# Kernel tuning notes

Measured on AMD Instinct MI355X. Metric: run time of the kernel, lower is better.

The kernel has to match this reference:

```python
import jax, jax.numpy as jnp
import numpy as np

H = 128          # hidden_size
GX = GY = 512    # grid_size
SW = 2           # spatial_width
NX = GX + 3 * SW # memory extent x (as in SpatialExternalMemory ctor)
NY = GY + 3 * SW
B = 512          # batch (num trajectories)
T = 64           # seq len (recurrent steps)


def setup_inputs() -> dict:
    key = jax.random.key(0)
    ks = jax.random.split(key, 9)
    stdv = 1.0 / np.sqrt(H)
    feat = jax.random.normal(ks[0], (B, T, 2), jnp.float32)
    # integer grid coords stored as floats in cols 2:4 (cast to long in forward)
    coords = jax.random.randint(ks[1], (B, T, 2), 0, GX).astype(jnp.float32)
    feature_tensor = jnp.concatenate([feat, coords], axis=-1)  # [B, T, 4]
    seq_lengths = jax.random.randint(ks[2], (B,), 1, T + 1)
    uni = lambda k, shp: jax.random.uniform(k, shp, jnp.float32, -stdv, stdv)
    return {
        "feature_tensor": feature_tensor,
        "W_ih": uni(ks[3], (4 * H, 2)),
        "b_ih": uni(ks[4], (4 * H,)),
        "W_hh": uni(ks[5], (4 * H, H)),
        "b_hh": uni(ks[6], (4 * H,)),
        "W_out": uni(ks[7], (H, 2 * H)),   # Attention.linear_out: [H, 2H]
        "b_out": uni(ks[8], (H,)),
        "seq_lengths": seq_lengths,
    }


def reference(feature_tensor, W_ih, b_ih, W_hh, b_hh, W_out, b_out, seq_lengths):
    step_idx = jnp.maximum(seq_lengths.astype(jnp.int32), 1) - 1  # [B]
    offsets = jnp.arange(-SW, SW + 1)                              # [K], K=2*SW+1
    K = 2 * SW + 1
    memory0 = jnp.zeros((NX, NY, H), jnp.float32)
    hidden0 = jnp.zeros((B, H), jnp.float32)
    last0 = jnp.zeros((B, H), jnp.float32)

    def step(carry, inp):
        hidden, memory, last = carry
        xt, t = inp                                 # xt: [B,4]
        feat = xt[:, :2]
        grid = xt[:, 2:4].astype(jnp.int32) + SW    # [B,2]
        gi = feat @ W_ih.T + b_ih                   # [B,4H]
        gh = hidden @ W_hh.T + b_hh                 # [B,4H]
        i_r, i_i, i_n, i_s = jnp.split(gi, 4, axis=1)
        h_r, h_i, h_n, h_s = jnp.split(gh, 4, axis=1)
        resetgate = jax.nn.sigmoid(i_r + h_r)
        updategate = jax.nn.sigmoid(i_i + h_i)
        spatialgate = jax.nn.sigmoid(i_s + h_s)
        newgate = jnp.tanh(i_n + resetgate * h_n)
        # --- find_nearby_grids: 5x5 neighborhood gather ---
        gx = jnp.clip(grid[:, 0], 0, NX - 1)
        gy = jnp.clip(grid[:, 1], 0, NY - 1)
        xi = jnp.clip(gx[:, None] + offsets[None, :], 0, NX - 1)   # [B,K]
        yi = jnp.clip(gy[:, None] + offsets[None, :], 0, NY - 1)   # [B,K]
        xg = jnp.broadcast_to(xi[:, :, None], (B, K, K)).reshape(B, K * K)
        yg = jnp.broadcast_to(yi[:, None, :], (B, K, K)).reshape(B, K * K)
        context = memory[xg, yg]                    # [B, K*K, H]
        # --- Attention(newgate.detach(), context) ---
        q = jax.lax.stop_gradient(newgate)
        scores = jnp.einsum('bh,bkh->bk', q, context)
        scores = jnp.where(scores == 0.0, -jnp.inf, scores)
        attn = jax.nn.softmax(scores, axis=1)
        attn = jnp.where(jnp.isnan(attn), 0.0, attn)
        mix = jnp.einsum('bk,bkh->bh', attn, context)
        atten_cs = jnp.tanh(jnp.concatenate([mix, q], axis=-1) @ W_out.T + b_out)
        curr = newgate + spatialgate * atten_cs
        out = curr + updategate * (hidden - curr)
        # --- in-cell memory write (detached, training-mode path) ---
        sd = jax.lax.stop_gradient(spatialgate)
        od = jax.lax.stop_gradient(out)
        upd = sd * memory[gx, gy] + (1.0 - sd) * od
        memory = memory.at[gx, gy].set(upd)
        last = jnp.where((step_idx == t)[:, None], out, last)
        return (out, memory, last), None

    xs = (jnp.swapaxes(feature_tensor, 0, 1), jnp.arange(T))
    (_, _, last), _ = jax.lax.scan(step, (hidden0, memory0, last0), xs)
    return last
```

## Files before the change

### kernel.cpp

```cpp
#include <hip/hip_runtime.h>
#include <hip/hip_fp16.h>
#include <math.h>

#define Hc   128
#define Bc   512
#define Tc   64
#define NXc  518
#define NCELL (518*518)
#define NEV  (Bc*Tc)
#define SWc  2


__global__ void k_build(const float* __restrict__ feat, int* __restrict__ head,
                        int* __restrict__ nxt, int* __restrict__ cellxy) {
    int gid = blockIdx.x * 256 + threadIdx.x;
    if (gid >= NEV) return;
    int b = gid >> 6, t = gid & 63;
    int base = (b * Tc + t) * 4;
    int gx = (int)feat[base + 2] + SWc;
    int gy = (int)feat[base + 3] + SWc;
    gx = min(max(gx, 0), NXc - 1);
    gy = min(max(gy, 0), NXc - 1);
    int cell = gx * NXc + gy;
    int e = t * Bc + b;
    cellxy[e] = (gx << 16) | gy;
    int old = atomicExch(&head[cell], e);
    nxt[e] = old;
}

__global__ void k_resolve(const int* __restrict__ head, const int* __restrict__ nxt,
                          const int* __restrict__ cellxy, int* __restrict__ dep) {
    int gid = blockIdx.x * 256 + threadIdx.x;
    if (gid >= NEV * 25) return;
    int r = gid / 25, k = gid - r * 25;
    int t = r & 63, b = r >> 6;
    int e0 = t * Bc + b;
    int xy = cellxy[e0];
    int gx = xy >> 16, gy = xy & 0xffff;
    int cx = gx + (k / 5) - SWc, cy = gy + (k % 5) - SWc;
    cx = min(max(cx, 0), NXc - 1);
    cy = min(max(cy, 0), NXc - 1);
    int cell = cx * NXc + cy;
    int best = -1;
    for (int e = head[cell]; e >= 0; e = nxt[e])
        if ((e >> 9) < t && e > best) best = e;
    dep[r * 25 + k] = best;
}


#define LOG2E 1.4426950408889634f
__device__ __forceinline__ float fexp(float x)  { return __builtin_amdgcn_exp2f(x * LOG2E); }
__device__ __forceinline__ float fsig(float x)  { return __builtin_amdgcn_rcpf(1.f + fexp(-x)); }
__device__ __forceinline__ float ftanh(float x) { return 1.f - 2.f * __builtin_amdgcn_rcpf(1.f + fexp(2.f * x)); }

template <int CTRL>
__device__ __forceinline__ float dppadd(float x) {
    int t = __builtin_amdgcn_update_dpp(0, __float_as_int(x), CTRL, 0xF, 0xF, true);
    return x + __int_as_float(t);
}
template <int CTRL>
__device__ __forceinline__ float dppmax(float x) {
    int t = __builtin_amdgcn_update_dpp(0, __float_as_int(x), CTRL, 0xF, 0xF, true);
    return fmaxf(x, __int_as_float(t));
}
__device__ __forceinline__ float swz16(float x) {
    return __int_as_float(__builtin_amdgcn_ds_swizzle(__float_as_int(x), 0x401F));
}
__device__ __forceinline__ float redsum64(float d) {
    d = dppadd<0xB1>(d); d = dppadd<0x4E>(d);
    d = dppadd<0x141>(d); d = dppadd<0x140>(d);
    d += swz16(d);
    d += __shfl_xor(d, 32, 64);
    return d;
}

__device__ __forceinline__ void barlds() {
    asm volatile("" ::: "memory");
    __builtin_amdgcn_s_waitcnt(0xC07F);
    __builtin_amdgcn_s_barrier();
    asm volatile("" ::: "memory");
}


constexpr int LDS_FLOATS = 16512 + 256 + 1024 + 256 + 256 + 256 + 64 + 2048 + 512 + 16 + 128 + 256 + 128;
constexpr int LDS_BYTES  = LDS_FLOATS * 4;

__global__ void
__attribute__((amdgpu_flat_work_group_size(1024, 1024)))
__attribute__((amdgpu_waves_per_eu(4, 4)))
step_main(const float* __restrict__ feat, const float* __restrict__ Wih,
          const float* __restrict__ bih,  const float* __restrict__ Whh,
          const float* __restrict__ bhh,  const float* __restrict__ Wout,
          const float* __restrict__ bout, const int*   __restrict__ seq,
          const int*   __restrict__ dep,  float* __restrict__ vbuf,
          unsigned*    __restrict__ flags, float* __restrict__ dout) {
    extern __shared__ float lds[];
    __half2* WoutH = (__half2*)lds;
    float* hid   = lds + 16512;
    float* g     = hid   + 256;
    float* gin   = g     + 1024;
    float* ctr   = gin   + 256;
    float* qvL   = ctr   + 256;
    float* scor  = qvL   + 256;
    float* pmix  = scor  + 64;
    float* catL  = pmix  + 2048;
    float* fxy   = catL  + 512;
    float* boutL = fxy   + 16;
    float* updL  = boutL + 128;
    int*   depv  = (int*)(updL + 256);

    const int tid  = threadIdx.x;
    const int blk  = blockIdx.x;
    const int lane = tid & 63;
    const int w    = tid >> 6;
    const int wj   = w >> 3;
    const int ww   = w & 7;

    const int rp = tid >> 2;
    const int q  = tid & 3;
    const int r0 = 2 * rp, r1 = 2 * rp + 1;
    float4 wr0[8], wr1[8];
    {
        const float4* w0 = (const float4*)(Whh + (size_t)r0 * Hc);
        const float4* w1 = (const float4*)(Whh + (size_t)r1 * Hc);
        #pragma unroll
        for (int i = 0; i < 8; ++i) { wr0[i] = w0[q + 4 * i]; wr1[i] = w1[q + 4 * i]; }
    }
    #pragma unroll
    for (int i = 0; i < 8; ++i) {
        asm volatile("" : "+v"(wr0[i].x), "+v"(wr0[i].y), "+v"(wr0[i].z), "+v"(wr0[i].w));
        asm volatile("" : "+v"(wr1[i].x), "+v"(wr1[i].y), "+v"(wr1[i].z), "+v"(wr1[i].w));
    }
    const int jw = q & 1;
    const int rw = r0 + (q >> 1);
    const float bihr = bih[rw], bhhr = bhh[rw];
    const float wihA = Wih[rw * 2 + 0], wihB = Wih[rw * 2 + 1];
    const int chunk = rw >> 7;

    for (int i = tid; i < 128 * 128; i += 1024) {
        int r = i >> 7, c2 = i & 127;
        WoutH[r * 129 + c2] = __floats2half2_rn(Wout[r * 256 + 2 * c2],
                                                Wout[r * 256 + 2 * c2 + 1]);
    }
    if (tid < 128) boutL[tid] = bout[tid];
    if (tid < 256) hid[tid] = 0.f;
    if (tid < 8) { int j = tid >> 2, c = tid & 3;
                   fxy[tid] = feat[((size_t)(blk * 2 + j) * Tc + 0) * 4 + c]; }
    if (tid < 50) {
        int j = (tid >= 25), k = tid - j * 25;
        depv[tid] = dep[(((size_t)(blk * 2 + j)) * Tc + 0) * 25 + k];
    }
    const int s0 = max(seq[blk * 2 + 0], 1) - 1;
    const int s1 = max(seq[blk * 2 + 1], 1) - 1;
    __syncthreads();

    const float NEG_INF = -__builtin_inff();

    for (int t = 0; t < Tc; ++t) {
        const float* fx = fxy + (t & 1) * 8;
        int* depvCur = depv + (t & 1) * 64;
        int* depvNxt = depv + ((t + 1) & 1) * 64;

        if (t > 0 && (w == 0 || w == 2)) {
            int j = w >> 1;
            float2 u = *(const float2*)&updL[j * 128 + 2 * lane];
            unsigned long long raw; __builtin_memcpy(&raw, &u, 8);
            __hip_atomic_store((unsigned long long*)(vbuf +
                ((size_t)((t - 1) * Bc + blk * 2 + j)) * Hc + 2 * lane),
                raw, __ATOMIC_RELAXED, __HIP_MEMORY_SCOPE_AGENT);
        }
        const int mye = (lane < 25) ? depvCur[wj * 25 + lane] : -1;
        unsigned fpre = 1u;
        if (mye >= 0)
            fpre = __hip_atomic_load(&flags[mye], __ATOMIC_RELAXED,
                                     __HIP_MEMORY_SCOPE_AGENT);

        float a00 = 0.f, a01 = 0.f, a10 = 0.f, a11 = 0.f;
        {
            const float4* h0 = (const float4*)hid;
            const float4* h1 = (const float4*)(hid + 128);
            #pragma unroll
            for (int i = 0; i < 8; ++i) {
                float4 hv0 = h0[q + 4 * i], hv1 = h1[q + 4 * i];
                float4 w0 = wr0[i], w1 = wr1[i];
                a00 = fmaf(w0.x, hv0.x, fmaf(w0.y, hv0.y, fmaf(w0.z, hv0.z, fmaf(w0.w, hv0.w, a00))));
                a01 = fmaf(w1.x, hv0.x, fmaf(w1.y, hv0.y, fmaf(w1.z, hv0.z, fmaf(w1.w, hv0.w, a01))));
                a10 = fmaf(w0.x, hv1.x, fmaf(w0.y, hv1.y, fmaf(w0.z, hv1.z, fmaf(w0.w, hv1.w, a10))));
                a11 = fmaf(w1.x, hv1.x, fmaf(w1.y, hv1.y, fmaf(w1.z, hv1.z, fmaf(w1.w, hv1.w, a11))));
            }
        }
        a00 = dppadd<0x4E>(dppadd<0xB1>(a00));
        a01 = dppadd<0x4E>(dppadd<0xB1>(a01));
        a10 = dppadd<0x4E>(dppadd<0xB1>(a10));
        a11 = dppadd<0x4E>(dppadd<0xB1>(a11));
        {
            float mine = (q & 1) ? ((q >> 1) ? a11 : a10) : ((q >> 1) ? a01 : a00);
            float gi  = fmaf(wihA, fx[jw * 4 + 0], wihB * fx[jw * 4 + 1]);
            g[jw * 512 + rw] = mine + bhhr + ((chunk == 2) ? 0.f : (gi + bihr));
            if (chunk == 2) gin[jw * 128 + (rw & 127)] = gi + bihr;
        }
        if (tid >= 512 && tid < 562 && t + 1 < Tc) {
            int idx = tid - 512;
            int j = (idx >= 25), k = idx - j * 25;
            depvNxt[idx] = dep[(((size_t)(blk * 2 + j)) * Tc + (t + 1)) * 25 + k];
        }
        if (tid >= 960 && tid < 968 && t + 1 < Tc) {
            int idx = tid - 960, j = idx >> 2, c = idx & 3;
            fxy[((t + 1) & 1) * 8 + idx] =
                feat[((size_t)(blk * 2 + j) * Tc + (t + 1)) * 4 + c];
        }
        if (t > 0 && (w == 0 || w == 2)) {
            asm volatile("s_waitcnt vmcnt(0)" ::: "memory");
            if (lane == 0)
                __hip_atomic_store(&flags[(t - 1) * Bc + blk * 2 + (w >> 1)], 1u,
                                   __ATOMIC_RELAXED, __HIP_MEMORY_SCOPE_AGENT);
        }
        {
            bool pend = (mye >= 0) && (fpre == 0u);
            while (__any(pend)) {
                if (pend && __hip_atomic_load(&flags[mye], __ATOMIC_RELAXED,
                                              __HIP_MEMORY_SCOPE_AGENT) != 0u)
                    pend = false;
                if (__any(pend)) __builtin_amdgcn_s_sleep(1);
            }
        }
        asm volatile("" ::: "memory");
        float2 valk[4];
        int    evk[4];
        #pragma unroll
        for (int kk = 0; kk < 4; ++kk) {
            int k = ww + 8 * kk;
            evk[kk] = (k < 25) ? depvCur[wj * 25 + k] : -1;
            valk[kk] = make_float2(0.f, 0.f);
            if (evk[kk] >= 0)
                valk[kk] = *(const float2*)(vbuf + (size_t)evk[kk] * Hc + 2 * lane);
        }
        barlds();

        float q0, q1;
        {
            float2 gr2 = *(const float2*)&g[wj * 512 + 2 * lane];
            float2 gn2 = *(const float2*)&g[wj * 512 + 256 + 2 * lane];
            float2 gi2 = *(const float2*)&gin[wj * 128 + 2 * lane];
            q0 = ftanh(gi2.x + fsig(gr2.x) * gn2.x);
            q1 = ftanh(gi2.y + fsig(gr2.y) * gn2.y);
        }
        if (ww == 0) *(float2*)&qvL[wj * 128 + 2 * lane] = make_float2(q0, q1);
        if (ww == 4)
            *(float2*)&ctr[wj * 128 + 2 * lane] =
                (evk[1] >= 0) ? valk[1] : make_float2(0.f, 0.f);
        #pragma unroll
        for (int kk = 0; kk < 4; ++kk) {
            int k = ww + 8 * kk;
            if (k < 25) {
                float sc;
                if (evk[kk] >= 0) {
                    float d = fmaf(valk[kk].x, q0, valk[kk].y * q1);
                    d = redsum64(d);
                    sc = (d == 0.f) ? NEG_INF : d;
                } else sc = NEG_INF;
                if (lane == 0) scor[wj * 32 + k] = sc;
            }
        }
        barlds();

        {
            int k2 = lane & 31;
            float v = (k2 < 25) ? scor[wj * 32 + k2] : NEG_INF;
            float m = v;
            m = dppmax<0xB1>(m); m = dppmax<0x4E>(m);
            m = dppmax<0x141>(m); m = dppmax<0x140>(m);
            m = fmaxf(m, swz16(m));
            float a = 0.f;
            if (m != NEG_INF) {
                float p = (v == NEG_INF) ? 0.f : fexp(v - m);
                float s = p;
                s = dppadd<0xB1>(s); s = dppadd<0x4E>(s);
                s = dppadd<0x141>(s); s = dppadd<0x140>(s);
                s += swz16(s);
                a = p / s;
            }
            float pm0 = 0.f, pm1 = 0.f;
            #pragma unroll
            for (int kk = 0; kk < 4; ++kk) {
                int k = ww + 8 * kk;
                if (k < 25 && evk[kk] >= 0) {
                    float ak = __int_as_float(
                        __builtin_amdgcn_readlane(__float_as_int(a), k));
                    pm0 = fmaf(ak, valk[kk].x, pm0);
                    pm1 = fmaf(ak, valk[kk].y, pm1);
                }
            }
            *(float2*)&pmix[(wj * 8 + ww) * 128 + 2 * lane] = make_float2(pm0, pm1);
        }
        barlds();

        if (tid < 256) {
            int j = tid >> 7, h = tid & 127;
            float mix = 0.f;
            #pragma unroll
            for (int p = 0; p < 8; ++p) mix += pmix[(j * 8 + p) * 128 + h];
            catL[j * 256 + h] = mix;
            catL[j * 256 + 128 + h] = qvL[j * 128 + h];
        }
        barlds();

        {
            int oo = tid & 127, rep = tid >> 7;
            const __half2* wrow = WoutH + oo * 129 + rep * 16;
            const float4* c04 = (const float4*)(catL + rep * 32);
            const float4* c14 = (const float4*)(catL + 256 + rep * 32);
            float acc0 = 0.f, acc1 = 0.f;
            #pragma unroll
            for (int i = 0; i < 8; ++i) {
                __half2 wa = wrow[2 * i], wb = wrow[2 * i + 1];
                float wx = __low2float(wa), wy = __high2float(wa);
                float wz = __low2float(wb), wwv = __high2float(wb);
                float4 c0 = c04[i], c1 = c14[i];
                acc0 = fmaf(wx, c0.x, fmaf(wy, c0.y, fmaf(wz, c0.z, fmaf(wwv, c0.w, acc0))));
                acc1 = fmaf(wx, c1.x, fmaf(wy, c1.y, fmaf(wz, c1.z, fmaf(wwv, c1.w, acc1))));
            }
            pmix[rep * 128 + oo]       = acc0;
            pmix[(8 + rep) * 128 + oo] = acc1;
        }
        barlds();

        if (tid < 256) {
            int j = tid >> 7, h = tid & 127;
            float tot = boutL[h];
            #pragma unroll
            for (int p = 0; p < 8; ++p) tot += pmix[(j * 8 + p) * 128 + h];
            float at = ftanh(tot);
            float gr = g[j * 512 + h],       gu = g[j * 512 + 128 + h];
            float gn = g[j * 512 + 256 + h], gs = g[j * 512 + 384 + h];
            float rr = fsig(gr), uu = fsig(gu), ss = fsig(gs);
            float nn = ftanh(gin[j * 128 + h] + rr * gn);
            float hv = hid[j * 128 + h];
            float curr = fmaf(ss, at, nn);
            float outv = curr + uu * (hv - curr);
            hid[j * 128 + h] = outv;
            if (t < Tc - 1)
                updL[tid] = fmaf(ss, ctr[j * 128 + h], (1.f - ss) * outv);
            int sj = (j == 0) ? s0 : s1;
            if (sj == t) dout[(size_t)(blk * 2 + j) * Hc + h] = outv;
        }
        barlds();
    }
}


extern "C" void kernel_launch(void* const* d_in, const int* in_sizes, int n_in,
                              void* d_out, int out_size, void* d_ws, size_t ws_size,
                              hipStream_t stream) {
    const float* feat = (const float*)d_in[0];
    const float* Wih  = (const float*)d_in[1];
    const float* bih  = (const float*)d_in[2];
    const float* Whh  = (const float*)d_in[3];
    const float* bhh  = (const float*)d_in[4];
    const float* Wout = (const float*)d_in[5];
    const float* bout = (const float*)d_in[6];
    const int*   seq  = (const int*)d_in[7];

    char* ws = (char*)d_ws;
    size_t off = 0;
    auto carve = [&](size_t bytes) { char* p = ws + off; off += (bytes + 511) & ~(size_t)511; return p; };
    float*    vbuf   = (float*)   carve((size_t)NEV * Hc * 4);
    int*      head   = (int*)     carve((size_t)NCELL * 4);
    int*      nxt    = (int*)     carve((size_t)NEV * 4);
    int*      cellxy = (int*)     carve((size_t)NEV * 4);
    int*      dep    = (int*)     carve((size_t)NEV * 25 * 4);
    unsigned* flags  = (unsigned*)carve((size_t)NEV * 4);

    hipMemsetAsync(head, 0xFF, (size_t)NCELL * 4, stream);
    hipMemsetAsync(flags, 0, (size_t)NEV * 4, stream);

    k_build<<<(NEV + 255) / 256, 256, 0, stream>>>(feat, head, nxt, cellxy);
    k_resolve<<<(NEV * 25 + 255) / 256, 256, 0, stream>>>(head, nxt, cellxy, dep);

    hipFuncSetAttribute((const void*)step_main,
                        hipFuncAttributeMaxDynamicSharedMemorySize, LDS_BYTES);
    step_main<<<256, 1024, LDS_BYTES, stream>>>(feat, Wih, bih, Whh, bhh, Wout, bout,
                                                seq, dep, vbuf, flags, (float*)d_out);
}
```

Measured before the change: 459.1 us.

## Tag memory-update values with step counter to replace separate flag synchronization

Each published memory update now packs the float with a step tag in a 64-bit word, so consumers poll the data itself instead of a separate flag array. This removes the store-then-waitcnt-then-flag handshake and the extra flag load round trip. The output projection is reorganized so each wave computes 8 outputs with cross-lane reductions, and the mix partials are accumulated with LDS atomics, which eliminates two barriers and the pmix/qvL buffers. In exchange vbuf doubles in size and needs a full memset, and each published value is written with per-element 64-bit atomic stores.

```diff
diff --git a/kernel.cpp b/kernel.cpp
--- a/kernel.cpp
+++ b/kernel.cpp
@@ -81,8 +81,12 @@
     asm volatile("" ::: "memory");
 }
 
-
-constexpr int LDS_FLOATS = 16512 + 256 + 1024 + 256 + 256 + 256 + 64 + 2048 + 512 + 16 + 128 + 256 + 128;
+__device__ __forceinline__ unsigned long long gload(const unsigned long long* p) {
+    return __hip_atomic_load(p, __ATOMIC_RELAXED, __HIP_MEMORY_SCOPE_AGENT);
+}
+
+
+constexpr int LDS_FLOATS = 16512 + 256 + 1024 + 256 + 256 + 64 + 512 + 16 + 128 + 128;
 constexpr int LDS_BYTES  = LDS_FLOATS * 4;
 
 __global__ void
@@ -92,22 +96,19 @@
           const float* __restrict__ bih,  const float* __restrict__ Whh,
           const float* __restrict__ bhh,  const float* __restrict__ Wout,
           const float* __restrict__ bout, const int*   __restrict__ seq,
-          const int*   __restrict__ dep,  float* __restrict__ vbuf,
-          unsigned*    __restrict__ flags, float* __restrict__ dout) {
+          const int*   __restrict__ dep,  unsigned long long* __restrict__ vbuf,
+          float* __restrict__ dout) {
     extern __shared__ float lds[];
     __half2* WoutH = (__half2*)lds;
     float* hid   = lds + 16512;
     float* g     = hid   + 256;
     float* gin   = g     + 1024;
     float* ctr   = gin   + 256;
-    float* qvL   = ctr   + 256;
-    float* scor  = qvL   + 256;
-    float* pmix  = scor  + 64;
-    float* catL  = pmix  + 2048;
+    float* scor  = ctr   + 256;
+    float* catL  = scor  + 64;
     float* fxy   = catL  + 512;
     float* boutL = fxy   + 16;
-    float* updL  = boutL + 128;
-    int*   depv  = (int*)(updL + 256);
+    int*   depv  = (int*)(boutL + 128);
 
     const int tid  = threadIdx.x;
     const int blk  = blockIdx.x;
@@ -161,19 +162,17 @@
         int* depvCur = depv + (t & 1) * 64;
         int* depvNxt = depv + ((t + 1) & 1) * 64;
 
-        if (t > 0 && (w == 0 || w == 2)) {
-            int j = w >> 1;
-            float2 u = *(const float2*)&updL[j * 128 + 2 * lane];
-            unsigned long long raw; __builtin_memcpy(&raw, &u, 8);
-            __hip_atomic_store((unsigned long long*)(vbuf +
-                ((size_t)((t - 1) * Bc + blk * 2 + j)) * Hc + 2 * lane),
-                raw, __ATOMIC_RELAXED, __HIP_MEMORY_SCOPE_AGENT);
-        }
-        const int mye = (lane < 25) ? depvCur[wj * 25 + lane] : -1;
-        unsigned fpre = 1u;
-        if (mye >= 0)
-            fpre = __hip_atomic_load(&flags[mye], __ATOMIC_RELAXED,
-                                     __HIP_MEMORY_SCOPE_AGENT);
+        int evk[4]; unsigned long long g0[4], g1[4];
+        #pragma unroll
+        for (int kk = 0; kk < 4; ++kk) {
+            int k = ww + 8 * kk;
+            evk[kk] = (k < 25) ? depvCur[wj * 25 + k] : -1;
+            g0[kk] = 0; g1[kk] = 0;
+            if (evk[kk] >= 0) {
+                const unsigned long long* p = vbuf + ((size_t)evk[kk] << 7) + 2 * lane;
+                g0[kk] = gload(p); g1[kk] = gload(p + 1);
+            }
+        }
 
         float a00 = 0.f, a01 = 0.f, a10 = 0.f, a11 = 0.f;
         {
@@ -209,31 +208,34 @@
             fxy[((t + 1) & 1) * 8 + idx] =
                 feat[((size_t)(blk * 2 + j) * Tc + (t + 1)) * 4 + c];
         }
-        if (t > 0 && (w == 0 || w == 2)) {
-            asm volatile("s_waitcnt vmcnt(0)" ::: "memory");
-            if (lane == 0)
-                __hip_atomic_store(&flags[(t - 1) * Bc + blk * 2 + (w >> 1)], 1u,
-                                   __ATOMIC_RELAXED, __HIP_MEMORY_SCOPE_AGENT);
-        }
-        {
-            bool pend = (mye >= 0) && (fpre == 0u);
-            while (__any(pend)) {
-                if (pend && __hip_atomic_load(&flags[mye], __ATOMIC_RELAXED,
-                                              __HIP_MEMORY_SCOPE_AGENT) != 0u)
-                    pend = false;
-                if (__any(pend)) __builtin_amdgcn_s_sleep(1);
-            }
-        }
-        asm volatile("" ::: "memory");
-        float2 valk[4];
-        int    evk[4];
+        float2 valk[4]; bool pend[4];
         #pragma unroll
         for (int kk = 0; kk < 4; ++kk) {
-            int k = ww + 8 * kk;
-            evk[kk] = (k < 25) ? depvCur[wj * 25 + k] : -1;
-            valk[kk] = make_float2(0.f, 0.f);
-            if (evk[kk] >= 0)
-                valk[kk] = *(const float2*)(vbuf + (size_t)evk[kk] * Hc + 2 * lane);
+            pend[kk] = false; valk[kk] = make_float2(0.f, 0.f);
+            if (evk[kk] >= 0) {
+                unsigned exp = (unsigned)((evk[kk] >> 9) + 1);
+                valk[kk] = make_float2(__uint_as_float((unsigned)g0[kk]),
+                                       __uint_as_float((unsigned)g1[kk]));
+                pend[kk] = ((unsigned)(g0[kk] >> 32) != exp) ||
+                           ((unsigned)(g1[kk] >> 32) != exp);
+            }
+        }
+        while (__any(pend[0] | pend[1] | pend[2] | pend[3])) {
+            #pragma unroll
+            for (int kk = 0; kk < 4; ++kk) {
+                if (pend[kk]) {
+                    unsigned exp = (unsigned)((evk[kk] >> 9) + 1);
+                    const unsigned long long* p = vbuf + ((size_t)evk[kk] << 7) + 2 * lane;
+                    unsigned long long r0v = gload(p), r1v = gload(p + 1);
+                    if ((unsigned)(r0v >> 32) == exp && (unsigned)(r1v >> 32) == exp) {
+                        valk[kk] = make_float2(__uint_as_float((unsigned)r0v),
+                                               __uint_as_float((unsigned)r1v));
+                        pend[kk] = false;
+                    }
+                }
+            }
+            if (__any(pend[0] | pend[1] | pend[2] | pend[3]))
+                __builtin_amdgcn_s_sleep(1);
         }
         barlds();
 
@@ -245,7 +247,8 @@
             q0 = ftanh(gi2.x + fsig(gr2.x) * gn2.x);
             q1 = ftanh(gi2.y + fsig(gr2.y) * gn2.y);
         }
-        if (ww == 0) *(float2*)&qvL[wj * 128 + 2 * lane] = make_float2(q0, q1);
+        if (ww == 0) *(float2*)&catL[wj * 256 + 128 + 2 * lane] = make_float2(q0, q1);
+        if (ww == 1) *(float2*)&catL[wj * 256 + 2 * lane] = make_float2(0.f, 0.f);
         if (ww == 4)
             *(float2*)&ctr[wj * 128 + 2 * lane] =
                 (evk[1] >= 0) ? valk[1] : make_float2(0.f, 0.f);
@@ -280,69 +283,69 @@
                 s += swz16(s);
                 a = p / s;
             }
-            float pm0 = 0.f, pm1 = 0.f;
-            #pragma unroll
-            for (int kk = 0; kk < 4; ++kk) {
-                int k = ww + 8 * kk;
-                if (k < 25 && evk[kk] >= 0) {
-                    float ak = __int_as_float(
-                        __builtin_amdgcn_readlane(__float_as_int(a), k));
-                    pm0 = fmaf(ak, valk[kk].x, pm0);
-                    pm1 = fmaf(ak, valk[kk].y, pm1);
+            if ((evk[0] >= 0) | (evk[1] >= 0) | (evk[2] >= 0) | (evk[3] >= 0)) {
+                float pm0 = 0.f, pm1 = 0.f;
+                #pragma unroll
+                for (int kk = 0; kk < 4; ++kk) {
+                    int k = ww + 8 * kk;
+                    if (k < 25 && evk[kk] >= 0) {
+                        float ak = __int_as_float(
+                            __builtin_amdgcn_readlane(__float_as_int(a), k));
+                        pm0 = fmaf(ak, valk[kk].x, pm0);
+                        pm1 = fmaf(ak, valk[kk].y, pm1);
+                    }
                 }
-            }
-            *(float2*)&pmix[(wj * 8 + ww) * 128 + 2 * lane] = make_float2(pm0, pm1);
+                atomicAdd(&catL[wj * 256 + 2 * lane],     pm0);
+                atomicAdd(&catL[wj * 256 + 2 * lane + 1], pm1);
+            }
         }
         barlds();
 
-        if (tid < 256) {
-            int j = tid >> 7, h = tid & 127;
-            float mix = 0.f;
-            #pragma unroll
-            for (int p = 0; p < 8; ++p) mix += pmix[(j * 8 + p) * 128 + h];
-            catL[j * 256 + h] = mix;
-            catL[j * 256 + 128 + h] = qvL[j * 128 + h];
-        }
-        barlds();
-
-        {
-            int oo = tid & 127, rep = tid >> 7;
-            const __half2* wrow = WoutH + oo * 129 + rep * 16;
-            const float4* c04 = (const float4*)(catL + rep * 32);
-            const float4* c14 = (const float4*)(catL + 256 + rep * 32);
+        {
+            const int oi = lane & 7, p = lane >> 3;
+            const int oo = 8 * w + oi;
+            const __half2* wrow = WoutH + oo * 129 + p * 16;
+            const float4* cat4 = (const float4*)catL;
             float acc0 = 0.f, acc1 = 0.f;
             #pragma unroll
-            for (int i = 0; i < 8; ++i) {
-                __half2 wa = wrow[2 * i], wb = wrow[2 * i + 1];
+            for (int c = 0; c < 8; ++c) {
+                int cc = (c + p) & 7;
+                __half2 wa = wrow[2 * cc], wb = wrow[2 * cc + 1];
                 float wx = __low2float(wa), wy = __high2float(wa);
-                float wz = __low2float(wb), wwv = __high2float(wb);
-                float4 c0 = c04[i], c1 = c14[i];
-                acc0 = fmaf(wx, c0.x, fmaf(wy, c0.y, fmaf(wz, c0.z, fmaf(wwv, c0.w, acc0))));
-                acc1 = fmaf(wx, c1.x, fmaf(wy, c1.y, fmaf(wz, c1.z, fmaf(wwv, c1.w, acc1))));
-            }
-            pmix[rep * 128 + oo]       = acc0;
-            pmix[(8 + rep) * 128 + oo] = acc1;
-        }
-        barlds();
-
-        if (tid < 256) {
-            int j = tid >> 7, h = tid & 127;
-            float tot = boutL[h];
-            #pragma unroll
-            for (int p = 0; p < 8; ++p) tot += pmix[(j * 8 + p) * 128 + h];
-            float at = ftanh(tot);
-            float gr = g[j * 512 + h],       gu = g[j * 512 + 128 + h];
-            float gn = g[j * 512 + 256 + h], gs = g[j * 512 + 384 + h];
-            float rr = fsig(gr), uu = fsig(gu), ss = fsig(gs);
-            float nn = ftanh(gin[j * 128 + h] + rr * gn);
-            float hv = hid[j * 128 + h];
-            float curr = fmaf(ss, at, nn);
-            float outv = curr + uu * (hv - curr);
-            hid[j * 128 + h] = outv;
-            if (t < Tc - 1)
-                updL[tid] = fmaf(ss, ctr[j * 128 + h], (1.f - ss) * outv);
-            int sj = (j == 0) ? s0 : s1;
-            if (sj == t) dout[(size_t)(blk * 2 + j) * Hc + h] = outv;
+                float wz = __low2float(wb), wv = __high2float(wb);
+                float4 v0 = cat4[p * 8 + cc];
+                float4 v1 = cat4[64 + p * 8 + cc];
+                acc0 = fmaf(wx, v0.x, fmaf(wy, v0.y, fmaf(wz, v0.z, fmaf(wv, v0.w, acc0))));
+                acc1 = fmaf(wx, v1.x, fmaf(wy, v1.y, fmaf(wz, v1.z, fmaf(wv, v1.w, acc1))));
+            }
+            acc0 = dppadd<0x128>(acc0); acc0 += swz16(acc0); acc0 += __shfl_xor(acc0, 32, 64);
+            acc1 = dppadd<0x128>(acc1); acc1 += swz16(acc1); acc1 += __shfl_xor(acc1, 32, 64);
+            if (lane < 8) {
+                #pragma unroll
+                for (int j = 0; j < 2; ++j) {
+                    float tot = ((j == 0) ? acc0 : acc1) + boutL[oo];
+                    float at = ftanh(tot);
+                    float gr = g[j * 512 + oo],       gu = g[j * 512 + 128 + oo];
+                    float gn = g[j * 512 + 256 + oo], gs = g[j * 512 + 384 + oo];
+                    float rr = fsig(gr), uu = fsig(gu), ss = fsig(gs);
+                    float nn = ftanh(gin[j * 128 + oo] + rr * gn);
+                    float hv = hid[j * 128 + oo];
+                    float curr = fmaf(ss, at, nn);
+                    float outv = curr + uu * (hv - curr);
+                    hid[j * 128 + oo] = outv;
+                    if (t < Tc - 1) {
+                        float upd = fmaf(ss, ctr[j * 128 + oo], (1.f - ss) * outv);
+                        int e = t * Bc + blk * 2 + j;
+                        unsigned long long payload =
+                            ((unsigned long long)(unsigned)(t + 1) << 32) |
+                            (unsigned long long)__float_as_uint(upd);
+                        __hip_atomic_store(vbuf + ((size_t)e << 7) + oo, payload,
+                                           __ATOMIC_RELAXED, __HIP_MEMORY_SCOPE_AGENT);
+                    }
+                    int sj = (j == 0) ? s0 : s1;
+                    if (sj == t) dout[(size_t)(blk * 2 + j) * Hc + oo] = outv;
+                }
+            }
         }
         barlds();
     }
@@ -364,15 +367,14 @@
     char* ws = (char*)d_ws;
     size_t off = 0;
     auto carve = [&](size_t bytes) { char* p = ws + off; off += (bytes + 511) & ~(size_t)511; return p; };
-    float*    vbuf   = (float*)   carve((size_t)NEV * Hc * 4);
-    int*      head   = (int*)     carve((size_t)NCELL * 4);
-    int*      nxt    = (int*)     carve((size_t)NEV * 4);
-    int*      cellxy = (int*)     carve((size_t)NEV * 4);
-    int*      dep    = (int*)     carve((size_t)NEV * 25 * 4);
-    unsigned* flags  = (unsigned*)carve((size_t)NEV * 4);
-
+    unsigned long long* vbuf = (unsigned long long*)carve((size_t)NEV * Hc * 8);
+    int* head   = (int*)carve((size_t)NCELL * 4);
+    int* nxt    = (int*)carve((size_t)NEV * 4);
+    int* cellxy = (int*)carve((size_t)NEV * 4);
+    int* dep    = (int*)carve((size_t)NEV * 25 * 4);
+
+    hipMemsetAsync(vbuf, 0, (size_t)NEV * Hc * 8, stream);
     hipMemsetAsync(head, 0xFF, (size_t)NCELL * 4, stream);
-    hipMemsetAsync(flags, 0, (size_t)NEV * 4, stream);
 
     k_build<<<(NEV + 255) / 256, 256, 0, stream>>>(feat, head, nxt, cellxy);
     k_resolve<<<(NEV * 25 + 255) / 256, 256, 0, stream>>>(head, nxt, cellxy, dep);
@@ -380,5 +382,5 @@
     hipFuncSetAttribute((const void*)step_main,
                         hipFuncAttributeMaxDynamicSharedMemorySize, LDS_BYTES);
     step_main<<<256, 1024, LDS_BYTES, stream>>>(feat, Wih, bih, Whh, bhh, Wout, bout,
-                                                seq, dep, vbuf, flags, (float*)d_out);
-}
+                                                seq, dep, vbuf, (float*)d_out);
+}
```

New measurement: 933.0 us. 2.03x slower.

## Fuse attention mix and output projection phases, cutting per-step barriers

Applied to the files above, without the earlier changes.

Partial attention mixes are now accumulated straight into the concat buffer with LDS atomics instead of being staged in a separate buffer and summed later. The output projection is regrouped so each wave owns 8 output rows, with the K dimension split across lanes and reduced through DPP and swizzle. This lets the gate/update epilogue run in the same phase. Together these drop two block-wide barriers and two LDS staging buffers from every recurrent step. In exchange the code adds LDS atomics, a cross-lane reduction, and an epilogue that only 8 lanes per wave execute, which lowers parallelism in that stage.

```diff
diff --git a/kernel.cpp b/kernel.cpp
--- a/kernel.cpp
+++ b/kernel.cpp
@@ -82,7 +82,7 @@
 }
 
 
-constexpr int LDS_FLOATS = 16512 + 256 + 1024 + 256 + 256 + 256 + 64 + 2048 + 512 + 16 + 128 + 256 + 128;
+constexpr int LDS_FLOATS = 16512 + 256 + 1024 + 256 + 256 + 64 + 512 + 16 + 128 + 256 + 128;
 constexpr int LDS_BYTES  = LDS_FLOATS * 4;
 
 __global__ void
@@ -100,10 +100,8 @@
     float* g     = hid   + 256;
     float* gin   = g     + 1024;
     float* ctr   = gin   + 256;
-    float* qvL   = ctr   + 256;
-    float* scor  = qvL   + 256;
-    float* pmix  = scor  + 64;
-    float* catL  = pmix  + 2048;
+    float* scor  = ctr   + 256;
+    float* catL  = scor  + 64;
     float* fxy   = catL  + 512;
     float* boutL = fxy   + 16;
     float* updL  = boutL + 128;
@@ -245,7 +243,8 @@
             q0 = ftanh(gi2.x + fsig(gr2.x) * gn2.x);
             q1 = ftanh(gi2.y + fsig(gr2.y) * gn2.y);
         }
-        if (ww == 0) *(float2*)&qvL[wj * 128 + 2 * lane] = make_float2(q0, q1);
+        if (ww == 0) *(float2*)&catL[wj * 256 + 128 + 2 * lane] = make_float2(q0, q1);
+        if (ww == 1) *(float2*)&catL[wj * 256 + 2 * lane] = make_float2(0.f, 0.f);
         if (ww == 4)
             *(float2*)&ctr[wj * 128 + 2 * lane] =
                 (evk[1] >= 0) ? valk[1] : make_float2(0.f, 0.f);
@@ -280,69 +279,62 @@
                 s += swz16(s);
                 a = p / s;
             }
-            float pm0 = 0.f, pm1 = 0.f;
-            #pragma unroll
-            for (int kk = 0; kk < 4; ++kk) {
-                int k = ww + 8 * kk;
-                if (k < 25 && evk[kk] >= 0) {
-                    float ak = __int_as_float(
-                        __builtin_amdgcn_readlane(__float_as_int(a), k));
-                    pm0 = fmaf(ak, valk[kk].x, pm0);
-                    pm1 = fmaf(ak, valk[kk].y, pm1);
+            if ((evk[0] >= 0) | (evk[1] >= 0) | (evk[2] >= 0) | (evk[3] >= 0)) {
+                float pm0 = 0.f, pm1 = 0.f;
+                #pragma unroll
+                for (int kk = 0; kk < 4; ++kk) {
+                    int k = ww + 8 * kk;
+                    if (k < 25 && evk[kk] >= 0) {
+                        float ak = __int_as_float(
+                            __builtin_amdgcn_readlane(__float_as_int(a), k));
+                        pm0 = fmaf(ak, valk[kk].x, pm0);
+                        pm1 = fmaf(ak, valk[kk].y, pm1);
+                    }
                 }
-            }
-            *(float2*)&pmix[(wj * 8 + ww) * 128 + 2 * lane] = make_float2(pm0, pm1);
+                atomicAdd(&catL[wj * 256 + 2 * lane],     pm0);
+                atomicAdd(&catL[wj * 256 + 2 * lane + 1], pm1);
+            }
         }
         barlds();
 
-        if (tid < 256) {
-            int j = tid >> 7, h = tid & 127;
-            float mix = 0.f;
-            #pragma unroll
-            for (int p = 0; p < 8; ++p) mix += pmix[(j * 8 + p) * 128 + h];
-            catL[j * 256 + h] = mix;
-            catL[j * 256 + 128 + h] = qvL[j * 128 + h];
-        }
-        barlds();
-
-        {
-            int oo = tid & 127, rep = tid >> 7;
-            const __half2* wrow = WoutH + oo * 129 + rep * 16;
-            const float4* c04 = (const float4*)(catL + rep * 32);
-            const float4* c14 = (const float4*)(catL + 256 + rep * 32);
+        {
+            const int oi = lane & 7, p = lane >> 3;
+            const int oo = 8 * w + oi;
+            const __half2* wrow = WoutH + oo * 129 + p * 16;
+            const float4* cat4 = (const float4*)catL;
             float acc0 = 0.f, acc1 = 0.f;
             #pragma unroll
-            for (int i = 0; i < 8; ++i) {
-                __half2 wa = wrow[2 * i], wb = wrow[2 * i + 1];
+            for (int c = 0; c < 8; ++c) {
+                int cc = (c + p) & 7;
+                __half2 wa = wrow[2 * cc], wb = wrow[2 * cc + 1];
                 float wx = __low2float(wa), wy = __high2float(wa);
-                float wz = __low2float(wb), wwv = __high2float(wb);
-                float4 c0 = c04[i], c1 = c14[i];
-                acc0 = fmaf(wx, c0.x, fmaf(wy, c0.y, fmaf(wz, c0.z, fmaf(wwv, c0.w, acc0))));
-                acc1 = fmaf(wx, c1.x, fmaf(wy, c1.y, fmaf(wz, c1.z, fmaf(wwv, c1.w, acc1))));
-            }
-            pmix[rep * 128 + oo]       = acc0;
-            pmix[(8 + rep) * 128 + oo] = acc1;
-        }
-        barlds();
-
-        if (tid < 256) {
-            int j = tid >> 7, h = tid & 127;
-            float tot = boutL[h];
-            #pragma unroll
-            for (int p = 0; p < 8; ++p) tot += pmix[(j * 8 + p) * 128 + h];
-            float at = ftanh(tot);
-            float gr = g[j * 512 + h],       gu = g[j * 512 + 128 + h];
-            float gn = g[j * 512 + 256 + h], gs = g[j * 512 + 384 + h];
-            float rr = fsig(gr), uu = fsig(gu), ss = fsig(gs);
-            float nn = ftanh(gin[j * 128 + h] + rr * gn);
-            float hv = hid[j * 128 + h];
-            float curr = fmaf(ss, at, nn);
-            float outv = curr + uu * (hv - curr);
-            hid[j * 128 + h] = outv;
-            if (t < Tc - 1)
-                updL[tid] = fmaf(ss, ctr[j * 128 + h], (1.f - ss) * outv);
-            int sj = (j == 0) ? s0 : s1;
-            if (sj == t) dout[(size_t)(blk * 2 + j) * Hc + h] = outv;
+                float wz = __low2float(wb), wv = __high2float(wb);
+                float4 v0 = cat4[p * 8 + cc];
+                float4 v1 = cat4[64 + p * 8 + cc];
+                acc0 = fmaf(wx, v0.x, fmaf(wy, v0.y, fmaf(wz, v0.z, fmaf(wv, v0.w, acc0))));
+                acc1 = fmaf(wx, v1.x, fmaf(wy, v1.y, fmaf(wz, v1.z, fmaf(wv, v1.w, acc1))));
+            }
+            acc0 = dppadd<0x128>(acc0); acc0 += swz16(acc0); acc0 += __shfl_xor(acc0, 32, 64);
+            acc1 = dppadd<0x128>(acc1); acc1 += swz16(acc1); acc1 += __shfl_xor(acc1, 32, 64);
+            if (lane < 8) {
+                #pragma unroll
+                for (int j = 0; j < 2; ++j) {
+                    float tot = ((j == 0) ? acc0 : acc1) + boutL[oo];
+                    float at = ftanh(tot);
+                    float gr = g[j * 512 + oo],       gu = g[j * 512 + 128 + oo];
+                    float gn = g[j * 512 + 256 + oo], gs = g[j * 512 + 384 + oo];
+                    float rr = fsig(gr), uu = fsig(gu), ss = fsig(gs);
+                    float nn = ftanh(gin[j * 128 + oo] + rr * gn);
+                    float hv = hid[j * 128 + oo];
+                    float curr = fmaf(ss, at, nn);
+                    float outv = curr + uu * (hv - curr);
+                    hid[j * 128 + oo] = outv;
+                    if (t < Tc - 1)
+                        updL[j * 128 + oo] = fmaf(ss, ctr[j * 128 + oo], (1.f - ss) * outv);
+                    int sj = (j == 0) ? s0 : s1;
+                    if (sj == t) dout[(size_t)(blk * 2 + j) * Hc + oo] = outv;
+                }
+            }
         }
         barlds();
     }
```

New measurement: 504.1 us. 9.8% more time.
